# Optimization experiments

Hardware: AMD Instinct MI355X
Metric: run time of the kernel (lower is better)

The kernel has to match this reference:

```python
import jax, jax.numpy as jnp
import numpy as np

OUT_F, IN_F = 11008, 4096

def dequant_2bit(weight_packed, weight_ranges):
    # weight_packed: [G, group/4] byte values; weight_ranges: [G, 2] fp16 (min, max)
    p = weight_packed.astype(jnp.int32)
    # unpack interleaved 2-bit fields: element 4j+k <- (packed[:, j] >> 2k) & 3
    q = jnp.stack([p & 3, (p >> 2) & 3, (p >> 4) & 3, (p >> 6) & 3], axis=-1)
    q = q.reshape(p.shape[0], -1).astype(jnp.float32)  # [G, group]
    r = weight_ranges.astype(jnp.float32)
    x_min = r[:, 0:1]
    x_max = r[:, 1:2]
    w = (q / 3.0) * (x_max - x_min) + x_min
    return w.reshape(-1)[: OUT_F * IN_F].reshape(OUT_F, IN_F)

def setup_inputs() -> dict:
    key = jax.random.key(0)
    k1, k2, k3, k4 = jax.random.split(key, 4)
    G = OUT_F * IN_F // 128  # group_size=128 -> 352256 groups
    x = jax.random.normal(k1, (32, 4096), dtype=jnp.float32)
    weight_packed = jax.random.randint(k2, (G, 32), 0, 256, dtype=jnp.int32)
    # ranges: sorted so min <= max, stored fp16 like the torch buffer
    weight_ranges = jnp.sort(jax.random.normal(k3, (G, 2), dtype=jnp.float32), axis=-1).astype(jnp.float16) * 0.1
    bias = jax.random.normal(k4, (OUT_F,), dtype=jnp.float32) * 0.02
    return {"x": x, "weight_packed": weight_packed, "weight_ranges": weight_ranges, "bias": bias}

def reference(x, weight_packed, weight_ranges, bias):
    W = dequant_2bit(weight_packed, weight_ranges)  # [out, in] fp32
    return x @ W.T + bias.astype(jnp.float32)
```

## Files before the change

### kernel.cpp

```cpp
#include <hip/hip_runtime.h>
#include <hip/hip_bf16.h>
#include <hip/hip_fp16.h>

typedef __attribute__((ext_vector_type(8))) short short8;
typedef __attribute__((ext_vector_type(4))) float f32x4;

#define OUT_F  11008
#define IN_F   4096
#define BN     64
#define SPLITS 4
#define KSTEPS 8
#define NB     (OUT_F / BN)

static __device__ __forceinline__ uint pack2_bf16(float a, float b) {
    __hip_bfloat162 h = __float22bfloat162_rn(make_float2(a, b));
    uint u;
    __builtin_memcpy(&u, &h, 4);
    return u;
}

static __device__ __forceinline__ float bf16_to_f(ushort u) {
    return __uint_as_float(((uint)u) << 16);
}

static __device__ __forceinline__ uint2 dq4(int p, float xmin, float dd) {
    float w0 = fmaf((float)(p & 3), dd, xmin);
    float w1 = fmaf((float)((p >> 2) & 3), dd, xmin);
    float w2 = fmaf((float)((p >> 4) & 3), dd, xmin);
    float w3 = fmaf((float)((p >> 6) & 3), dd, xmin);
    return make_uint2(pack2_bf16(w0, w1), pack2_bf16(w2, w3));
}

static __device__ __forceinline__ void rng_decode(uint ru, float2 rf, int fmt,
                                                  float& xmin, float& dd) {
    float xmax;
    if (fmt == 2) {
        xmin = rf.x; xmax = rf.y;
    } else if (fmt == 1) {
        xmin = bf16_to_f((ushort)(ru & 0xffff));
        xmax = bf16_to_f((ushort)(ru >> 16));
    } else {
        __half2 h;
        __builtin_memcpy(&h, &ru, 4);
        xmin = __half2float(h.x); xmax = __half2float(h.y);
    }
    dd = (xmax - xmin) * (1.0f / 3.0f);
}

__global__ __launch_bounds__(256)
void prep_kernel(const float* __restrict__ bias, float* __restrict__ out) {
    const int i = blockIdx.x * 256 + threadIdx.x;
    const int m  = i / 2752;
    const int n4 = i % 2752;
    ((float4*)out)[m * 2752 + n4] = ((const float4*)bias)[n4];
}

__global__ __launch_bounds__(256, 3)
void gemm_kernel(const float* __restrict__ x,
                 const int* __restrict__ packed,
                 const void* __restrict__ rr,
                 float* __restrict__ out) {
    const int nb   = blockIdx.x;
    const int s    = blockIdx.y;
    const int t    = threadIdx.x;
    const int lane = t & 63;
    const int wv   = t >> 6;

    __shared__ __align__(16) char wtile[BN * 256];
    __shared__ __align__(16) char atile[32 * 256];
    __shared__ int s_viol[3];
    __shared__ int s_max[3];
    __shared__ int s_fmt;

    if (t < 3) { s_viol[t] = 0; s_max[t] = 0; }
    __syncthreads();
    {
        const int g = 1024 + t;
        const uint   ru = ((const uint*)rr)[g];
        const float2 rf = ((const float2*)rr)[g];
        int viol[3]; float mx[3];
        {
            __half2 h; __builtin_memcpy(&h, &ru, 4);
            const float a = __half2float(h.x), c = __half2float(h.y);
            viol[0] = !(fabsf(a) < 1.f && fabsf(c) < 1.f && a <= c);
            mx[0] = fabsf(c);
        }
        {
            const float a = bf16_to_f((ushort)(ru & 0xffff));
            const float c = bf16_to_f((ushort)(ru >> 16));
            viol[1] = !(fabsf(a) < 1.f && fabsf(c) < 1.f && a <= c);
            mx[1] = fabsf(c);
        }
        {
            viol[2] = !(fabsf(rf.x) < 1.f && fabsf(rf.y) < 1.f && rf.x <= rf.y);
            mx[2] = fabsf(rf.y);
        }
#pragma unroll
        for (int h = 0; h < 3; ++h) {
            if (viol[h]) atomicOr(&s_viol[h], 1);
            atomicMax(&s_max[h], __float_as_int(mx[h]));
        }
    }
    __syncthreads();
    if (t == 0) {
        const float lo = 0.02f;
        int f = 0;
        if      (!s_viol[2] && __int_as_float(s_max[2]) > lo) f = 2;
        else if (!s_viol[1] && __int_as_float(s_max[1]) > lo) f = 1;
        s_fmt = f;
    }
    __syncthreads();
    const int fmt = s_fmt;

    const int i4  = t & 7;
    const int nr0 = t >> 3;
    const int n0  = nb * BN + nr0;
    const int n1  = n0 + 32;
    const int kb0 = s * KSTEPS;
    const int* pb0 = packed + n0 * 1024 + i4 * 4;
    const int* pb1 = packed + n1 * 1024 + i4 * 4;

    const float* xsrc = x + (t >> 3) * IN_F + (t & 7) * 16;
    char* adst = atile + (t >> 3) * 256;
    const uint aswz = (uint)(((t >> 3) & 7) << 4);

    const char* asrc0 = atile + (lane & 15) * 256;
    const char* asrc1 = atile + ((lane & 15) + 16) * 256;
    const uint  arsw  = (uint)((lane & 7) << 4);

    f32x4 acc0 = {0.f, 0.f, 0.f, 0.f};
    f32x4 acc1 = {0.f, 0.f, 0.f, 0.f};

    int4  p4c0 = *(const int4*)(pb0 + kb0 * 32);
    int4  p4c1 = *(const int4*)(pb1 + kb0 * 32);
    uint  ruc0 = 0, ruc1 = 0;
    float2 rfc0 = {0.f, 0.f}, rfc1 = {0.f, 0.f};
    if (fmt == 2) {
        rfc0 = ((const float2*)rr)[n0 * 32 + kb0];
        rfc1 = ((const float2*)rr)[n1 * 32 + kb0];
    } else {
        ruc0 = ((const uint*)rr)[n0 * 32 + kb0];
        ruc1 = ((const uint*)rr)[n1 * 32 + kb0];
    }

    for (int step = 0; step < KSTEPS; ++step) {
        const int kb = kb0 + step;
        const int k0 = kb << 7;

        float4 xf0 = *(const float4*)(xsrc + k0);
        float4 xf1 = *(const float4*)(xsrc + k0 + 4);
        float4 xf2 = *(const float4*)(xsrc + k0 + 8);
        float4 xf3 = *(const float4*)(xsrc + k0 + 12);

        __syncthreads();

        int4 p4n0, p4n1;
        uint run0 = 0, run1 = 0;
        float2 rfn0, rfn1;
        if (step + 1 < KSTEPS) {
            const int kn = kb + 1;
            p4n0 = *(const int4*)(pb0 + kn * 32);
            p4n1 = *(const int4*)(pb1 + kn * 32);
            if (fmt == 2) {
                rfn0 = ((const float2*)rr)[n0 * 32 + kn];
                rfn1 = ((const float2*)rr)[n1 * 32 + kn];
            } else {
                run0 = ((const uint*)rr)[n0 * 32 + kn];
                run1 = ((const uint*)rr)[n1 * 32 + kn];
            }
        }

        {
            uint q0 = pack2_bf16(xf0.x, xf0.y), q1 = pack2_bf16(xf0.z, xf0.w);
            uint q2 = pack2_bf16(xf1.x, xf1.y), q3 = pack2_bf16(xf1.z, xf1.w);
            uint q4 = pack2_bf16(xf2.x, xf2.y), q5 = pack2_bf16(xf2.z, xf2.w);
            uint q6 = pack2_bf16(xf3.x, xf3.y), q7 = pack2_bf16(xf3.z, xf3.w);
            const uint cb = (uint)((t & 7) * 32);
            *(uint4*)(adst + (cb ^ aswz))        = make_uint4(q0, q1, q2, q3);
            *(uint4*)(adst + ((cb + 16) ^ aswz)) = make_uint4(q4, q5, q6, q7);
        }

        {
            float xmin, dd;
            rng_decode(ruc0, rfc0, fmt, xmin, dd);
            char* dst = wtile + nr0 * 256;
            const uint swz = (uint)((nr0 & 7) << 4);
            uint2 q0 = dq4(p4c0.x, xmin, dd);
            uint2 q1 = dq4(p4c0.y, xmin, dd);
            *(uint4*)(dst + (uint)((32 * i4) ^ swz)) = make_uint4(q0.x, q0.y, q1.x, q1.y);
            uint2 q2 = dq4(p4c0.z, xmin, dd);
            uint2 q3 = dq4(p4c0.w, xmin, dd);
            *(uint4*)(dst + (uint)((32 * i4 + 16) ^ swz)) = make_uint4(q2.x, q2.y, q3.x, q3.y);
        }
        {
            float xmin, dd;
            rng_decode(ruc1, rfc1, fmt, xmin, dd);
            const int nr = nr0 + 32;
            char* dst = wtile + nr * 256;
            const uint swz = (uint)((nr & 7) << 4);
            uint2 q0 = dq4(p4c1.x, xmin, dd);
            uint2 q1 = dq4(p4c1.y, xmin, dd);
            *(uint4*)(dst + (uint)((32 * i4) ^ swz)) = make_uint4(q0.x, q0.y, q1.x, q1.y);
            uint2 q2 = dq4(p4c1.z, xmin, dd);
            uint2 q3 = dq4(p4c1.w, xmin, dd);
            *(uint4*)(dst + (uint)((32 * i4 + 16) ^ swz)) = make_uint4(q2.x, q2.y, q3.x, q3.y);
        }
        __syncthreads();

        const int  nrow = (wv << 4) | (lane & 15);
        const char* bsrc = wtile + nrow * 256;
        const uint bswz = (uint)((nrow & 7) << 4);
#pragma unroll
        for (int kc = 0; kc < 4; ++kc) {
            const uint cb = (uint)((kc << 6) | ((lane >> 4) << 4));
            short8 av0 = *(const short8*)(asrc0 + (cb ^ arsw));
            short8 av1 = *(const short8*)(asrc1 + (cb ^ arsw));
            short8 bf  = *(const short8*)(bsrc  + (cb ^ bswz));
            acc0 = __builtin_amdgcn_mfma_f32_16x16x32_bf16(av0, bf, acc0, 0, 0, 0);
            acc1 = __builtin_amdgcn_mfma_f32_16x16x32_bf16(av1, bf, acc1, 0, 0, 0);
        }

        if (step + 1 < KSTEPS) {
            p4c0 = p4n0; p4c1 = p4n1;
            ruc0 = run0; ruc1 = run1;
            rfc0 = rfn0; rfc1 = rfn1;
        }
    }

    const int col = nb * BN + (wv << 4) + (lane & 15);
    const int r0  = (lane >> 4) << 2;
#pragma unroll
    for (int v = 0; v < 4; ++v) {
        atomicAdd(out + (r0 + v) * OUT_F + col,        acc0[v]);
        atomicAdd(out + (16 + r0 + v) * OUT_F + col,   acc1[v]);
    }
}

extern "C" void kernel_launch(void* const* d_in, const int* in_sizes, int n_in,
                              void* d_out, int out_size, void* d_ws, size_t ws_size,
                              hipStream_t stream) {
    const float* x      = (const float*)d_in[0];
    const int*   packed = (const int*)d_in[1];
    const void*  rr     = (const void*)d_in[2];
    const float* bias   = (const float*)d_in[3];
    float*       out    = (float*)d_out;
    (void)d_ws; (void)ws_size;

    prep_kernel<<<344, 256, 0, stream>>>(bias, out);
    gemm_kernel<<<dim3(NB, SPLITS), 256, 0, stream>>>(x, packed, rr, out);
}
```

Measured before the change: 35.59 us.

## Double-buffer LDS tiles, prefetch x, and replace atomics with split-K partials reduction

```diff
diff --git a/kernel.cpp b/kernel.cpp
--- a/kernel.cpp
+++ b/kernel.cpp
@@ -11,6 +11,8 @@
 #define SPLITS 4
 #define KSTEPS 8
 #define NB     (OUT_F / BN)
+#define WBYTES (BN * 256)
+#define BUFSZ  (WBYTES + 32 * 256)
 
 static __device__ __forceinline__ uint pack2_bf16(float a, float b) {
     __hip_bfloat162 h = __float22bfloat162_rn(make_float2(a, b));
@@ -47,27 +49,18 @@
     dd = (xmax - xmin) * (1.0f / 3.0f);
 }
 
-__global__ __launch_bounds__(256)
-void prep_kernel(const float* __restrict__ bias, float* __restrict__ out) {
-    const int i = blockIdx.x * 256 + threadIdx.x;
-    const int m  = i / 2752;
-    const int n4 = i % 2752;
-    ((float4*)out)[m * 2752 + n4] = ((const float4*)bias)[n4];
-}
-
 __global__ __launch_bounds__(256, 3)
 void gemm_kernel(const float* __restrict__ x,
                  const int* __restrict__ packed,
                  const void* __restrict__ rr,
-                 float* __restrict__ out) {
+                 float* __restrict__ part) {
     const int nb   = blockIdx.x;
     const int s    = blockIdx.y;
     const int t    = threadIdx.x;
     const int lane = t & 63;
     const int wv   = t >> 6;
 
-    __shared__ __align__(16) char wtile[BN * 256];
-    __shared__ __align__(16) char atile[32 * 256];
+    __shared__ __align__(16) char lds[2 * BUFSZ];
     __shared__ int s_viol[3];
     __shared__ int s_max[3];
     __shared__ int s_fmt;
@@ -119,14 +112,15 @@
     const int kb0 = s * KSTEPS;
     const int* pb0 = packed + n0 * 1024 + i4 * 4;
     const int* pb1 = packed + n1 * 1024 + i4 * 4;
+    const uint*   rr_u  = (const uint*)rr;
+    const float2* rr_f2 = (const float2*)rr;
 
     const float* xsrc = x + (t >> 3) * IN_F + (t & 7) * 16;
-    char* adst = atile + (t >> 3) * 256;
     const uint aswz = (uint)(((t >> 3) & 7) << 4);
-
-    const char* asrc0 = atile + (lane & 15) * 256;
-    const char* asrc1 = atile + ((lane & 15) + 16) * 256;
-    const uint  arsw  = (uint)((lane & 7) << 4);
+    const uint acb  = (uint)((t & 7) * 32);
+
+    const int  ar0  = (lane & 15);
+    const uint arsw = (uint)((lane & 7) << 4);
 
     f32x4 acc0 = {0.f, 0.f, 0.f, 0.f};
     f32x4 acc1 = {0.f, 0.f, 0.f, 0.f};
@@ -136,54 +130,61 @@
     uint  ruc0 = 0, ruc1 = 0;
     float2 rfc0 = {0.f, 0.f}, rfc1 = {0.f, 0.f};
     if (fmt == 2) {
-        rfc0 = ((const float2*)rr)[n0 * 32 + kb0];
-        rfc1 = ((const float2*)rr)[n1 * 32 + kb0];
+        rfc0 = rr_f2[n0 * 32 + kb0];
+        rfc1 = rr_f2[n1 * 32 + kb0];
     } else {
-        ruc0 = ((const uint*)rr)[n0 * 32 + kb0];
-        ruc1 = ((const uint*)rr)[n1 * 32 + kb0];
+        ruc0 = rr_u[n0 * 32 + kb0];
+        ruc1 = rr_u[n1 * 32 + kb0];
+    }
+    float4 xc0, xc1, xc2, xc3;
+    {
+        const float* xs = xsrc + (kb0 << 7);
+        xc0 = *(const float4*)(xs);
+        xc1 = *(const float4*)(xs + 4);
+        xc2 = *(const float4*)(xs + 8);
+        xc3 = *(const float4*)(xs + 12);
     }
 
     for (int step = 0; step < KSTEPS; ++step) {
-        const int kb = kb0 + step;
-        const int k0 = kb << 7;
-
-        float4 xf0 = *(const float4*)(xsrc + k0);
-        float4 xf1 = *(const float4*)(xsrc + k0 + 4);
-        float4 xf2 = *(const float4*)(xsrc + k0 + 8);
-        float4 xf3 = *(const float4*)(xsrc + k0 + 12);
-
-        __syncthreads();
+        char* const wt = lds + (step & 1) * BUFSZ;
+        char* const at = wt + WBYTES;
 
         int4 p4n0, p4n1;
         uint run0 = 0, run1 = 0;
-        float2 rfn0, rfn1;
+        float2 rfn0 = {0.f, 0.f}, rfn1 = {0.f, 0.f};
+        float4 xn0, xn1, xn2, xn3;
         if (step + 1 < KSTEPS) {
-            const int kn = kb + 1;
+            const int kn = kb0 + step + 1;
             p4n0 = *(const int4*)(pb0 + kn * 32);
             p4n1 = *(const int4*)(pb1 + kn * 32);
             if (fmt == 2) {
-                rfn0 = ((const float2*)rr)[n0 * 32 + kn];
-                rfn1 = ((const float2*)rr)[n1 * 32 + kn];
+                rfn0 = rr_f2[n0 * 32 + kn];
+                rfn1 = rr_f2[n1 * 32 + kn];
             } else {
-                run0 = ((const uint*)rr)[n0 * 32 + kn];
-                run1 = ((const uint*)rr)[n1 * 32 + kn];
+                run0 = rr_u[n0 * 32 + kn];
+                run1 = rr_u[n1 * 32 + kn];
             }
-        }
-
-        {
-            uint q0 = pack2_bf16(xf0.x, xf0.y), q1 = pack2_bf16(xf0.z, xf0.w);
-            uint q2 = pack2_bf16(xf1.x, xf1.y), q3 = pack2_bf16(xf1.z, xf1.w);
-            uint q4 = pack2_bf16(xf2.x, xf2.y), q5 = pack2_bf16(xf2.z, xf2.w);
-            uint q6 = pack2_bf16(xf3.x, xf3.y), q7 = pack2_bf16(xf3.z, xf3.w);
-            const uint cb = (uint)((t & 7) * 32);
-            *(uint4*)(adst + (cb ^ aswz))        = make_uint4(q0, q1, q2, q3);
-            *(uint4*)(adst + ((cb + 16) ^ aswz)) = make_uint4(q4, q5, q6, q7);
+            const float* xs = xsrc + (kn << 7);
+            xn0 = *(const float4*)(xs);
+            xn1 = *(const float4*)(xs + 4);
+            xn2 = *(const float4*)(xs + 8);
+            xn3 = *(const float4*)(xs + 12);
+        }
+
+        {
+            uint q0 = pack2_bf16(xc0.x, xc0.y), q1 = pack2_bf16(xc0.z, xc0.w);
+            uint q2 = pack2_bf16(xc1.x, xc1.y), q3 = pack2_bf16(xc1.z, xc1.w);
+            uint q4 = pack2_bf16(xc2.x, xc2.y), q5 = pack2_bf16(xc2.z, xc2.w);
+            uint q6 = pack2_bf16(xc3.x, xc3.y), q7 = pack2_bf16(xc3.z, xc3.w);
+            char* adst = at + (t >> 3) * 256;
+            *(uint4*)(adst + (acb ^ aswz))        = make_uint4(q0, q1, q2, q3);
+            *(uint4*)(adst + ((acb + 16) ^ aswz)) = make_uint4(q4, q5, q6, q7);
         }
 
         {
             float xmin, dd;
             rng_decode(ruc0, rfc0, fmt, xmin, dd);
-            char* dst = wtile + nr0 * 256;
+            char* dst = wt + nr0 * 256;
             const uint swz = (uint)((nr0 & 7) << 4);
             uint2 q0 = dq4(p4c0.x, xmin, dd);
             uint2 q1 = dq4(p4c0.y, xmin, dd);
@@ -196,7 +197,7 @@
             float xmin, dd;
             rng_decode(ruc1, rfc1, fmt, xmin, dd);
             const int nr = nr0 + 32;
-            char* dst = wtile + nr * 256;
+            char* dst = wt + nr * 256;
             const uint swz = (uint)((nr & 7) << 4);
             uint2 q0 = dq4(p4c1.x, xmin, dd);
             uint2 q1 = dq4(p4c1.y, xmin, dd);
@@ -205,35 +206,60 @@
             uint2 q3 = dq4(p4c1.w, xmin, dd);
             *(uint4*)(dst + (uint)((32 * i4 + 16) ^ swz)) = make_uint4(q2.x, q2.y, q3.x, q3.y);
         }
-        __syncthreads();
-
-        const int  nrow = (wv << 4) | (lane & 15);
-        const char* bsrc = wtile + nrow * 256;
-        const uint bswz = (uint)((nrow & 7) << 4);
-#pragma unroll
-        for (int kc = 0; kc < 4; ++kc) {
-            const uint cb = (uint)((kc << 6) | ((lane >> 4) << 4));
-            short8 av0 = *(const short8*)(asrc0 + (cb ^ arsw));
-            short8 av1 = *(const short8*)(asrc1 + (cb ^ arsw));
-            short8 bf  = *(const short8*)(bsrc  + (cb ^ bswz));
-            acc0 = __builtin_amdgcn_mfma_f32_16x16x32_bf16(av0, bf, acc0, 0, 0, 0);
-            acc1 = __builtin_amdgcn_mfma_f32_16x16x32_bf16(av1, bf, acc1, 0, 0, 0);
+
+        asm volatile("s_waitcnt lgkmcnt(0)" ::: "memory");
+        __builtin_amdgcn_s_barrier();
+        __builtin_amdgcn_sched_barrier(0);
+
+        {
+            const char* asrc0 = at + ar0 * 256;
+            const char* asrc1 = at + (ar0 + 16) * 256;
+            const int  nrow = (wv << 4) | (lane & 15);
+            const char* bsrc = wt + nrow * 256;
+            const uint bswz = (uint)((nrow & 7) << 4);
+#pragma unroll
+            for (int kc = 0; kc < 4; ++kc) {
+                const uint cb = (uint)((kc << 6) | ((lane >> 4) << 4));
+                short8 av0 = *(const short8*)(asrc0 + (cb ^ arsw));
+                short8 av1 = *(const short8*)(asrc1 + (cb ^ arsw));
+                short8 bf  = *(const short8*)(bsrc  + (cb ^ bswz));
+                acc0 = __builtin_amdgcn_mfma_f32_16x16x32_bf16(av0, bf, acc0, 0, 0, 0);
+                acc1 = __builtin_amdgcn_mfma_f32_16x16x32_bf16(av1, bf, acc1, 0, 0, 0);
+            }
         }
 
         if (step + 1 < KSTEPS) {
             p4c0 = p4n0; p4c1 = p4n1;
             ruc0 = run0; ruc1 = run1;
             rfc0 = rfn0; rfc1 = rfn1;
-        }
-    }
-
+            xc0 = xn0; xc1 = xn1; xc2 = xn2; xc3 = xn3;
+        }
+    }
+
+    float* pout = part + (size_t)s * (32 * OUT_F);
     const int col = nb * BN + (wv << 4) + (lane & 15);
     const int r0  = (lane >> 4) << 2;
 #pragma unroll
     for (int v = 0; v < 4; ++v) {
-        atomicAdd(out + (r0 + v) * OUT_F + col,        acc0[v]);
-        atomicAdd(out + (16 + r0 + v) * OUT_F + col,   acc1[v]);
-    }
+        pout[(r0 + v) * OUT_F + col]      = acc0[v];
+        pout[(16 + r0 + v) * OUT_F + col] = acc1[v];
+    }
+}
+
+__global__ __launch_bounds__(256)
+void reduce_kernel(const float* __restrict__ part,
+                   const float* __restrict__ bias,
+                   float* __restrict__ out) {
+    const int i = blockIdx.x * 256 + threadIdx.x;
+    const int n4 = i % 2752;
+    const float4* p4 = (const float4*)part;
+    float4 a = ((const float4*)bias)[n4];
+#pragma unroll
+    for (int ss = 0; ss < SPLITS; ++ss) {
+        const float4 v = p4[ss * 88064 + i];
+        a.x += v.x; a.y += v.y; a.z += v.z; a.w += v.w;
+    }
+    ((float4*)out)[i] = a;
 }
 
 extern "C" void kernel_launch(void* const* d_in, const int* in_sizes, int n_in,
@@ -244,8 +270,8 @@
     const void*  rr     = (const void*)d_in[2];
     const float* bias   = (const float*)d_in[3];
     float*       out    = (float*)d_out;
-    (void)d_ws; (void)ws_size;
-
-    prep_kernel<<<344, 256, 0, stream>>>(bias, out);
-    gemm_kernel<<<dim3(NB, SPLITS), 256, 0, stream>>>(x, packed, rr, out);
-}
+    float*       part   = (float*)d_ws;
+
+    gemm_kernel<<<dim3(NB, SPLITS), 256, 0, stream>>>(x, packed, rr, part);
+    reduce_kernel<<<344, 256, 0, stream>>>(part, bias, out);
+}
```

Measured after the change: 31.76 us. 10.8% less time.
